# Kernel optimization log

Hardware: AMD Instinct MI355X
Metric: run time of the kernel (lower is better)

The kernel has to match this reference:

```python
import jax, jax.numpy as jnp
import numpy as np

IN_FEATURES = 4096
OUT_FEATURES = 12288
GROUP_SIZE = 128
NUM_GROUPS = (IN_FEATURES + GROUP_SIZE - 1) // GROUP_SIZE  # 32
PADDED_IN = NUM_GROUPS * GROUP_SIZE  # 4096 (no padding needed here)


def setup_inputs() -> dict:
    key = jax.random.key(0)
    kx, kq, ks, kb = jax.random.split(key, 4)
    x = jax.random.normal(kx, (8, 32, IN_FEATURES), dtype=jnp.float16)
    # int8 quantized weight in [-128, 127]
    weight_q = jax.random.randint(kq, (OUT_FEATURES, PADDED_IN), -128, 128, dtype=jnp.int32).astype(jnp.int8)
    # positive per-(row, group) symmetric scales, fp16, clamped >= 1e-8 as in load_from_float_weight
    scales = (jax.random.uniform(ks, (OUT_FEATURES, NUM_GROUPS), dtype=jnp.float32) * 0.01 + 1e-4).astype(jnp.float16)
    bias = (jax.random.normal(kb, (OUT_FEATURES,), dtype=jnp.float32) * 0.02).astype(jnp.float16)
    return {"x": x, "scales": scales, "bias": bias, "weight_q": weight_q}


def reference(x, scales, bias, weight_q):
    # Dequantize: [O, P] int8 -> [O, G, gs] fp16, scaled per (row, group)
    compute_dtype = jnp.float16
    q3 = weight_q.astype(compute_dtype).reshape(OUT_FEATURES, NUM_GROUPS, GROUP_SIZE)
    w = (q3 * scales.astype(compute_dtype)[:, :, None]).reshape(OUT_FEATURES, PADDED_IN)[:, :IN_FEATURES]
    # F.linear: y = x @ w.T + b
    out = jnp.einsum('bsi,oi->bso', x, w) + bias.astype(compute_dtype)
    return out
```

## Files before the change

### kernel.cpp

```cpp
#include <hip/hip_runtime.h>

typedef _Float16 h16x8 __attribute__((ext_vector_type(8)));
typedef _Float16 h16x4 __attribute__((ext_vector_type(4)));
typedef float    f32x4 __attribute__((ext_vector_type(4)));

#define NDIM   12288
#define KDIM   4096
#define MDIM   256
#define N_TILE 48
#define NT     32

__global__ __launch_bounds__(256) void cvt_x_kernel(const float* __restrict__ x,
                                                    _Float16* __restrict__ xf) {
    int i = blockIdx.x * 256 + threadIdx.x;
    f32x4 v = *(const f32x4*)(x + (size_t)i * 4);
    h16x4 h;
    h[0] = (_Float16)v[0]; h[1] = (_Float16)v[1];
    h[2] = (_Float16)v[2]; h[3] = (_Float16)v[3];
    *(h16x4*)(xf + (size_t)i * 4) = h;
}

template<int USE_F16X>
__global__ __launch_bounds__(512) void qlin_kernel(
    const float*    __restrict__ xf32,
    const _Float16* __restrict__ xf16,
    const float*    __restrict__ scales,
    const float*    __restrict__ bias,
    const int*      __restrict__ wq,
    float*          __restrict__ out)
{
    __shared__ char  wl[2][N_TILE * 256];
    __shared__ float sc[N_TILE * 32];

    const int tid  = threadIdx.x;
    const int lane = tid & 63;
    const int wave = tid >> 6;
    const int n0   = blockIdx.x * N_TILE;

    for (int j = tid; j < N_TILE * 32; j += 512)
        sc[j] = scales[(size_t)(n0 + (j >> 5)) * 32 + (j & 31)];

    const int r0    = tid >> 5;
    const int kc    = (tid & 31) * 4;
    const int xorw  = (r0 & 7) << 4;
    const int wbyte = ((tid & 31) * 8) ^ xorw;

    const int* wp0 = wq + (size_t)(n0 + r0     ) * KDIM + kc;
    const int* wp1 = wq + (size_t)(n0 + r0 + 16) * KDIM + kc;
    const int* wp2 = wq + (size_t)(n0 + r0 + 32) * KDIM + kc;

    int4 q0 = *(const int4*)wp0;
    int4 q1 = *(const int4*)wp1;
    int4 q2 = *(const int4*)wp2;

    __syncthreads();

    auto cvt_write = [&](int buf, int g) {
        float s0 = sc[(r0     ) * 32 + g];
        float s1 = sc[(r0 + 16) * 32 + g];
        float s2 = sc[(r0 + 32) * 32 + g];
        h16x4 h;
        h[0] = (_Float16)((float)q0.x * s0); h[1] = (_Float16)((float)q0.y * s0);
        h[2] = (_Float16)((float)q0.z * s0); h[3] = (_Float16)((float)q0.w * s0);
        *(h16x4*)(&wl[buf][(r0     ) * 256 + wbyte]) = h;
        h[0] = (_Float16)((float)q1.x * s1); h[1] = (_Float16)((float)q1.y * s1);
        h[2] = (_Float16)((float)q1.z * s1); h[3] = (_Float16)((float)q1.w * s1);
        *(h16x4*)(&wl[buf][(r0 + 16) * 256 + wbyte]) = h;
        h[0] = (_Float16)((float)q2.x * s2); h[1] = (_Float16)((float)q2.y * s2);
        h[2] = (_Float16)((float)q2.z * s2); h[3] = (_Float16)((float)q2.w * s2);
        *(h16x4*)(&wl[buf][(r0 + 32) * 256 + wbyte]) = h;
    };

    cvt_write(0, 0);

    const int arow = lane & 15;
    const int g16  = lane >> 4;
    const size_t idx0 = (size_t)(wave * 32 + arow) * KDIM + g16 * 8;
    const int xorv = (arow & 7) << 4;

    auto load_a = [&](size_t idx) -> h16x8 {
        if constexpr (USE_F16X) {
            return *(const h16x8*)(xf16 + idx);
        } else {
            f32x4 u0 = *(const f32x4*)(xf32 + idx);
            f32x4 u1 = *(const f32x4*)(xf32 + idx + 4);
            h16x8 a;
            a[0] = (_Float16)u0[0]; a[1] = (_Float16)u0[1];
            a[2] = (_Float16)u0[2]; a[3] = (_Float16)u0[3];
            a[4] = (_Float16)u1[0]; a[5] = (_Float16)u1[1];
            a[6] = (_Float16)u1[2]; a[7] = (_Float16)u1[3];
            return a;
        }
    };

    f32x4 zero = {0.f, 0.f, 0.f, 0.f};
    f32x4 acc[2][3];
    #pragma unroll
    for (int i = 0; i < 2; ++i)
        #pragma unroll
        for (int j = 0; j < 3; ++j) acc[i][j] = zero;

    __syncthreads();

    int cur = 0;
    for (int t = 0; t < NT; ++t) {
        if (t + 1 < NT) {
            q0 = *(const int4*)(wp0 + (t + 1) * 128);
            q1 = *(const int4*)(wp1 + (t + 1) * 128);
            q2 = *(const int4*)(wp2 + (t + 1) * 128);
        }
        const char* wb = wl[cur];
        #pragma unroll
        for (int kk = 0; kk < 4; ++kk) {
            h16x8 a0 = load_a(idx0 + t * 128 + kk * 32);
            h16x8 a1 = load_a(idx0 + (size_t)16 * KDIM + t * 128 + kk * 32);
            #pragma unroll
            for (int ni = 0; ni < 3; ++ni) {
                h16x8 b = *(const h16x8*)(wb + (ni * 16 + arow) * 256
                                             + ((kk * 64 + g16 * 16) ^ xorv));
                acc[0][ni] = __builtin_amdgcn_mfma_f32_16x16x32_f16(a0, b, acc[0][ni], 0, 0, 0);
                acc[1][ni] = __builtin_amdgcn_mfma_f32_16x16x32_f16(a1, b, acc[1][ni], 0, 0, 0);
            }
        }
        if (t + 1 < NT) cvt_write(cur ^ 1, t + 1);
        __syncthreads();
        cur ^= 1;
    }

    float bv0 = bias[n0 + arow];
    float bv1 = bias[n0 + 16 + arow];
    float bv2 = bias[n0 + 32 + arow];
    #pragma unroll
    for (int mi = 0; mi < 2; ++mi) {
        #pragma unroll
        for (int r = 0; r < 4; ++r) {
            int m = wave * 32 + mi * 16 + g16 * 4 + r;
            float* op = out + (size_t)m * NDIM + n0 + arow;
            op[0]  = acc[mi][0][r] + bv0;
            op[16] = acc[mi][1][r] + bv1;
            op[32] = acc[mi][2][r] + bv2;
        }
    }
}

extern "C" void kernel_launch(void* const* d_in, const int* in_sizes, int n_in,
                              void* d_out, int out_size, void* d_ws, size_t ws_size,
                              hipStream_t stream) {
    const float* x      = (const float*)d_in[0];
    const float* scales = (const float*)d_in[1];
    const float* bias   = (const float*)d_in[2];
    const int*   wq     = (const int*)d_in[3];
    float*       out    = (float*)d_out;

    const size_t xf_bytes = (size_t)MDIM * KDIM * sizeof(_Float16);
    if (ws_size >= xf_bytes) {
        _Float16* xf = (_Float16*)d_ws;
        cvt_x_kernel<<<dim3(MDIM * KDIM / 1024), dim3(256), 0, stream>>>(x, xf);
        qlin_kernel<1><<<dim3(NDIM / N_TILE), dim3(512), 0, stream>>>(x, xf, scales, bias, wq, out);
    } else {
        qlin_kernel<0><<<dim3(NDIM / N_TILE), dim3(512), 0, stream>>>(x, nullptr, scales, bias, wq, out);
    }
}
```

Measured before the change: 327.5 us.

## Use 1024-thread blocks with per-wave 16-row tiles and deeper weight prefetch

Doubles the block to 16 waves, so each wave now owns 16 rows of M instead of 32. This halves the per-wave accumulators and raises the number of waves in flight to hide memory latency. Weight loading is remapped so each wave reads one output row per slot with coalesced int2 loads. The main loop is unrolled by two with register prefetch two tiles ahead, which deepens the global-load pipeline. In exchange, each LDS B fragment is reused by only one A fragment per wave, which raises LDS read traffic, and more threads must synchronise at every barrier.

```diff
diff --git a/kernel.cpp b/kernel.cpp
--- a/kernel.cpp
+++ b/kernel.cpp
@@ -2,6 +2,7 @@
 
 typedef _Float16 h16x8 __attribute__((ext_vector_type(8)));
 typedef _Float16 h16x4 __attribute__((ext_vector_type(4)));
+typedef _Float16 h16x2 __attribute__((ext_vector_type(2)));
 typedef float    f32x4 __attribute__((ext_vector_type(4)));
 
 #define NDIM   12288
@@ -21,7 +22,7 @@
 }
 
 template<int USE_F16X>
-__global__ __launch_bounds__(512) void qlin_kernel(
+__global__ __launch_bounds__(1024, 4) void qlin_kernel(
     const float*    __restrict__ xf32,
     const _Float16* __restrict__ xf16,
     const float*    __restrict__ scales,
@@ -37,46 +38,34 @@
     const int wave = tid >> 6;
     const int n0   = blockIdx.x * N_TILE;
 
-    for (int j = tid; j < N_TILE * 32; j += 512)
+    for (int j = tid; j < N_TILE * 32; j += 1024)
         sc[j] = scales[(size_t)(n0 + (j >> 5)) * 32 + (j & 31)];
 
-    const int r0    = tid >> 5;
-    const int kc    = (tid & 31) * 4;
-    const int xorw  = (r0 & 7) << 4;
-    const int wbyte = ((tid & 31) * 8) ^ xorw;
+    const int2* wb0 = (const int2*)wq + (size_t)(n0 + wave     ) * 2048 + lane;
+    const int2* wb1 = (const int2*)wq + (size_t)(n0 + wave + 16) * 2048 + lane;
+    const int2* wb2 = (const int2*)wq + (size_t)(n0 + wave + 32) * 2048 + lane;
+    const int xors  = (wave & 7) << 4;
+    const int wby0  = (wave     ) * 256 + ((lane * 4) ^ xors);
+    const int wby1  = (wave + 16) * 256 + ((lane * 4) ^ xors);
+    const int wby2  = (wave + 32) * 256 + ((lane * 4) ^ xors);
 
-    const int* wp0 = wq + (size_t)(n0 + r0     ) * KDIM + kc;
-    const int* wp1 = wq + (size_t)(n0 + r0 + 16) * KDIM + kc;
-    const int* wp2 = wq + (size_t)(n0 + r0 + 32) * KDIM + kc;
-
-    int4 q0 = *(const int4*)wp0;
-    int4 q1 = *(const int4*)wp1;
-    int4 q2 = *(const int4*)wp2;
-
-    __syncthreads();
-
-    auto cvt_write = [&](int buf, int g) {
-        float s0 = sc[(r0     ) * 32 + g];
-        float s1 = sc[(r0 + 16) * 32 + g];
-        float s2 = sc[(r0 + 32) * 32 + g];
-        h16x4 h;
-        h[0] = (_Float16)((float)q0.x * s0); h[1] = (_Float16)((float)q0.y * s0);
-        h[2] = (_Float16)((float)q0.z * s0); h[3] = (_Float16)((float)q0.w * s0);
-        *(h16x4*)(&wl[buf][(r0     ) * 256 + wbyte]) = h;
-        h[0] = (_Float16)((float)q1.x * s1); h[1] = (_Float16)((float)q1.y * s1);
-        h[2] = (_Float16)((float)q1.z * s1); h[3] = (_Float16)((float)q1.w * s1);
-        *(h16x4*)(&wl[buf][(r0 + 16) * 256 + wbyte]) = h;
-        h[0] = (_Float16)((float)q2.x * s2); h[1] = (_Float16)((float)q2.y * s2);
-        h[2] = (_Float16)((float)q2.z * s2); h[3] = (_Float16)((float)q2.w * s2);
-        *(h16x4*)(&wl[buf][(r0 + 32) * 256 + wbyte]) = h;
+    auto cw = [&](int buf, int g, int2 a, int2 b, int2 c) {
+        float s0 = sc[(wave     ) * 32 + g];
+        float s1 = sc[(wave + 16) * 32 + g];
+        float s2 = sc[(wave + 32) * 32 + g];
+        h16x2 h;
+        h[0] = (_Float16)((float)a.x * s0); h[1] = (_Float16)((float)a.y * s0);
+        *(h16x2*)(&wl[buf][wby0]) = h;
+        h[0] = (_Float16)((float)b.x * s1); h[1] = (_Float16)((float)b.y * s1);
+        *(h16x2*)(&wl[buf][wby1]) = h;
+        h[0] = (_Float16)((float)c.x * s2); h[1] = (_Float16)((float)c.y * s2);
+        *(h16x2*)(&wl[buf][wby2]) = h;
     };
-
-    cvt_write(0, 0);
 
     const int arow = lane & 15;
     const int g16  = lane >> 4;
-    const size_t idx0 = (size_t)(wave * 32 + arow) * KDIM + g16 * 8;
     const int xorv = (arow & 7) << 4;
+    const size_t aidx0 = (size_t)(wave * 16 + arow) * KDIM + g16 * 8;
 
     auto load_a = [&](size_t idx) -> h16x8 {
         if constexpr (USE_F16X) {
@@ -93,53 +82,54 @@
         }
     };
 
-    f32x4 zero = {0.f, 0.f, 0.f, 0.f};
-    f32x4 acc[2][3];
-    #pragma unroll
-    for (int i = 0; i < 2; ++i)
+    f32x4 acc0 = {0.f,0.f,0.f,0.f}, acc1 = acc0, acc2 = acc0;
+
+    auto mfma_phase = [&](int t, int buf) {
+        const char* wbp = wl[buf];
         #pragma unroll
-        for (int j = 0; j < 3; ++j) acc[i][j] = zero;
+        for (int kk = 0; kk < 4; ++kk) {
+            h16x8 a = load_a(aidx0 + t * 128 + kk * 32);
+            h16x8 b0 = *(const h16x8*)(wbp + (      arow) * 256 + ((kk * 64 + g16 * 16) ^ xorv));
+            h16x8 b1 = *(const h16x8*)(wbp + (16  + arow) * 256 + ((kk * 64 + g16 * 16) ^ xorv));
+            h16x8 b2 = *(const h16x8*)(wbp + (32  + arow) * 256 + ((kk * 64 + g16 * 16) ^ xorv));
+            acc0 = __builtin_amdgcn_mfma_f32_16x16x32_f16(a, b0, acc0, 0, 0, 0);
+            acc1 = __builtin_amdgcn_mfma_f32_16x16x32_f16(a, b1, acc1, 0, 0, 0);
+            acc2 = __builtin_amdgcn_mfma_f32_16x16x32_f16(a, b2, acc2, 0, 0, 0);
+        }
+    };
 
+    int2 qA0 = wb0[0],   qA1 = wb1[0],   qA2 = wb2[0];
+    __syncthreads();
+    cw(0, 0, qA0, qA1, qA2);
+    qA0 = wb0[64];  qA1 = wb1[64];  qA2 = wb2[64];
+    int2 qB0 = wb0[128], qB1 = wb1[128], qB2 = wb2[128];
     __syncthreads();
 
-    int cur = 0;
-    for (int t = 0; t < NT; ++t) {
-        if (t + 1 < NT) {
-            q0 = *(const int4*)(wp0 + (t + 1) * 128);
-            q1 = *(const int4*)(wp1 + (t + 1) * 128);
-            q2 = *(const int4*)(wp2 + (t + 1) * 128);
+    for (int t = 0; t < NT; t += 2) {
+        mfma_phase(t, 0);
+        cw(1, t + 1, qA0, qA1, qA2);
+        if (t + 3 < NT) {
+            qA0 = wb0[(t + 3) * 64]; qA1 = wb1[(t + 3) * 64]; qA2 = wb2[(t + 3) * 64];
         }
-        const char* wb = wl[cur];
-        #pragma unroll
-        for (int kk = 0; kk < 4; ++kk) {
-            h16x8 a0 = load_a(idx0 + t * 128 + kk * 32);
-            h16x8 a1 = load_a(idx0 + (size_t)16 * KDIM + t * 128 + kk * 32);
-            #pragma unroll
-            for (int ni = 0; ni < 3; ++ni) {
-                h16x8 b = *(const h16x8*)(wb + (ni * 16 + arow) * 256
-                                             + ((kk * 64 + g16 * 16) ^ xorv));
-                acc[0][ni] = __builtin_amdgcn_mfma_f32_16x16x32_f16(a0, b, acc[0][ni], 0, 0, 0);
-                acc[1][ni] = __builtin_amdgcn_mfma_f32_16x16x32_f16(a1, b, acc[1][ni], 0, 0, 0);
-            }
+        __syncthreads();
+        mfma_phase(t + 1, 1);
+        if (t + 2 < NT) cw(0, t + 2, qB0, qB1, qB2);
+        if (t + 4 < NT) {
+            qB0 = wb0[(t + 4) * 64]; qB1 = wb1[(t + 4) * 64]; qB2 = wb2[(t + 4) * 64];
         }
-        if (t + 1 < NT) cvt_write(cur ^ 1, t + 1);
         __syncthreads();
-        cur ^= 1;
     }
 
-    float bv0 = bias[n0 + arow];
+    float bv0 = bias[n0 +      arow];
     float bv1 = bias[n0 + 16 + arow];
     float bv2 = bias[n0 + 32 + arow];
     #pragma unroll
-    for (int mi = 0; mi < 2; ++mi) {
-        #pragma unroll
-        for (int r = 0; r < 4; ++r) {
-            int m = wave * 32 + mi * 16 + g16 * 4 + r;
-            float* op = out + (size_t)m * NDIM + n0 + arow;
-            op[0]  = acc[mi][0][r] + bv0;
-            op[16] = acc[mi][1][r] + bv1;
-            op[32] = acc[mi][2][r] + bv2;
-        }
+    for (int r = 0; r < 4; ++r) {
+        int m = wave * 16 + g16 * 4 + r;
+        float* op = out + (size_t)m * NDIM + n0 + arow;
+        op[0]  = acc0[r] + bv0;
+        op[16] = acc1[r] + bv1;
+        op[32] = acc2[r] + bv2;
     }
 }
 
@@ -156,8 +146,8 @@
     if (ws_size >= xf_bytes) {
         _Float16* xf = (_Float16*)d_ws;
         cvt_x_kernel<<<dim3(MDIM * KDIM / 1024), dim3(256), 0, stream>>>(x, xf);
-        qlin_kernel<1><<<dim3(NDIM / N_TILE), dim3(512), 0, stream>>>(x, xf, scales, bias, wq, out);
+        qlin_kernel<1><<<dim3(NDIM / N_TILE), dim3(1024), 0, stream>>>(x, xf, scales, bias, wq, out);
     } else {
-        qlin_kernel<0><<<dim3(NDIM / N_TILE), dim3(512), 0, stream>>>(x, nullptr, scales, bias, wq, out);
+        qlin_kernel<0><<<dim3(NDIM / N_TILE), dim3(1024), 0, stream>>>(x, nullptr, scales, bias, wq, out);
     }
 }
```

Result: faster. 312.5 us (-4.6%).
